# Kernel optimization log

Measured on AMD Instinct MI355X. Metric: run time of the kernel, lower is better.

## Reference

```python
import jax, jax.numpy as jnp
import numpy as np

KATZ = 0.5      # katz_factor
GAMMA = 20.0    # support->query softmax temperature
GAMMA2 = 10.0   # query->support softmax temperature
EPS = 1e-16


def setup_inputs() -> dict:
    key = jax.random.key(0)
    k1, k2 = jax.random.split(key)
    support_xf = jax.random.normal(k1, (4, 25, 640, 10, 10), dtype=jnp.float32)
    query_xf = jax.random.normal(k2, (4, 75, 640, 10, 10), dtype=jnp.float32)
    return {"support_xf": support_xf, "query_xf": query_xf, "n_way": 5, "k_shot": 5}


def reference(support_xf, query_xf, n_way, k_shot):
    b, s, c, h, w = support_xf.shape
    q = query_xf.shape[1]
    M = h * w
    # mean over shots -> class prototypes per spatial location
    sup = support_xf.reshape(b, n_way, k_shot, c, M).mean(axis=2)   # (b, n, c, M)
    qry = query_xf.reshape(b, q, c, M)                               # (b, q, c, M)
    # cosine similarity: l2-normalize along channel dim
    sup = sup / (EPS + jnp.linalg.norm(sup, axis=2, keepdims=True))
    qry = qry / (EPS + jnp.linalg.norm(qry, axis=2, keepdims=True))
    # S[b,q,m,n,s] = <qry[b,q,:,m], sup[b,n,:,s]>  (matches permute(0,1,3,2,4))
    S = jnp.einsum('bqcm,bncs->bqmns', qry, sup)
    M_q = M
    M_s = n_way * M
    N = b * q
    S = S.reshape(N, M_q, M_s)
    # bipartite transition matrices (row-stochastic softmaxes)
    T_sq = jax.nn.softmax(GAMMA * S, axis=-1)                        # (N, M_q, M_s)
    T_qs = jax.nn.softmax(GAMMA2 * jnp.swapaxes(S, -2, -1), axis=-1)  # (N, M_s, M_q)
    D = M_s + M_q
    zs = jnp.zeros((N, M_s, M_s), S.dtype)
    zq = jnp.zeros((N, M_q, M_q), S.dtype)
    top = jnp.concatenate([zs, jnp.swapaxes(T_sq, -2, -1)], axis=-1)   # (N, M_s, D)
    bot = jnp.concatenate([jnp.swapaxes(T_qs, -2, -1), zq], axis=-1)   # (N, M_q, D)
    T = jnp.concatenate([top, bot], axis=-2)                           # (N, D, D)
    # katz = (inv(I - k*T) - I) @ 1  ==  solve(I - k*T, 1) - 1
    A = jnp.eye(D, dtype=S.dtype)[None] - KATZ * T
    katz = jnp.linalg.solve(A, jnp.ones((N, D, 1), S.dtype))[..., 0] - 1.0
    kq = katz[:, M_s:]
    kq = kq / kq.sum(axis=-1, keepdims=True)
    return kq.reshape(b, q, h, w)[:, :, None]  # (b, q, 1, h, w)
```

## Files before the change

kernel.cpp:

```cpp
#include <hip/hip_runtime.h>
#include <math.h>

#define BATCH 4
#define NSUP 25
#define NQ   75
#define CH   640
#define HW   100
#define NWAY 5
#define KSHOT 5
#define NSYS (BATCH*NQ)
#define MS   (NWAY*HW)
#define MQ   HW
#define MTOT (NQ*HW)
#define NCHK 20

#define A_BSTRIDE 241664
#define A_KSTRIDE 966656
#define B_BSTRIDE 16384
#define B_KSTRIDE 65536

typedef __attribute__((ext_vector_type(8))) _Float16 f16x8;
typedef __attribute__((ext_vector_type(8))) short bf16x8;
typedef __attribute__((ext_vector_type(4))) float f32x4;
typedef __attribute__((ext_vector_type(16))) float f32x16;
typedef __attribute__((ext_vector_type(4))) short s16x4;

__device__ __forceinline__ ushort f2bf(float f) {
    unsigned u = __float_as_uint(f);
    u += 0x7fff + ((u >> 16) & 1);
    return (ushort)(u >> 16);
}
__device__ __forceinline__ ushort f2h(float f) {
    _Float16 h = (_Float16)f;
    return __builtin_bit_cast(unsigned short, h);
}

#define GLD_LDS16(gp, lp) __builtin_amdgcn_global_load_lds( \
    (const __attribute__((address_space(1))) unsigned*)(const void*)(gp), \
    (__attribute__((address_space(3))) unsigned*)(void*)(lp), 16, 0, 0)

__global__ __launch_bounds__(256) void k_prep_all(
        const float* __restrict__ qry, const float* __restrict__ sup,
        ushort* __restrict__ AhT, ushort* __restrict__ BhT,
        float* __restrict__ npq, float* __restrict__ nps) {
    __shared__ float tile[32][101];
    int kt = blockIdx.x;
    int c0 = kt * 32;
    int z  = blockIdx.y;
    int t  = threadIdx.x;
    bool isq = (z < BATCH*NQ);

    ushort* dst; float* normpart; int planesHW; size_t cbase; int brow; int p;
    if (isq) {
        p = z;
        int b = p / NQ, qq = p % NQ;
        dst = AhT; normpart = npq; planesHW = NSYS*HW;
        cbase = (size_t)kt*A_KSTRIDE + (size_t)b*A_BSTRIDE;
        brow = qq*100;
        const float* ib = qry + (size_t)p*CH*HW + (size_t)c0*HW;
#pragma unroll
        for (int ii = 0; ii < 4; ++ii) {
            int idx = ii*256 + t;
            if (idx < 800) {
                int cl = idx / 25, qd = idx % 25;
                float4 v = *(const float4*)(ib + idx*4);
                tile[cl][qd*4+0] = v.x; tile[cl][qd*4+1] = v.y;
                tile[cl][qd*4+2] = v.z; tile[cl][qd*4+3] = v.w;
            }
        }
    } else {
        p = z - BATCH*NQ;
        int b = p / NWAY, n = p % NWAY;
        dst = BhT; normpart = nps; planesHW = BATCH*NWAY*HW;
        cbase = (size_t)kt*B_KSTRIDE + (size_t)b*B_BSTRIDE;
        brow = n*100;
        const float* ib = sup + ((size_t)(b*NSUP + n*KSHOT))*CH*HW + (size_t)c0*HW;
#pragma unroll
        for (int ii = 0; ii < 4; ++ii) {
            int idx = ii*256 + t;
            if (idx < 800) {
                float4 a = {0.f,0.f,0.f,0.f};
#pragma unroll
                for (int k = 0; k < KSHOT; ++k) {
                    float4 w = *(const float4*)(ib + (size_t)k*CH*HW + idx*4);
                    a.x += w.x; a.y += w.y; a.z += w.z; a.w += w.w;
                }
                int cl = idx / 25, qd = idx % 25;
                tile[cl][qd*4+0] = a.x*0.2f; tile[cl][qd*4+1] = a.y*0.2f;
                tile[cl][qd*4+2] = a.z*0.2f; tile[cl][qd*4+3] = a.w*0.2f;
            }
        }
    }
    __syncthreads();
#pragma unroll
    for (int ii = 0; ii < 2; ++ii) {
        int idx = ii*256 + t;
        if (idx < 400) {
            int m  = idx >> 2;
            int sp = idx & 3;
            int rib = brow + m;
            int rl = rib & 127;
            int slab = rib >> 7;
            int cb = ((sp ^ ((rl >> 1) & 3))) << 3;
            bf16x8 o; float ss = 0.f;
#pragma unroll
            for (int j = 0; j < 8; ++j) {
                float f = tile[cb+j][m];
                ss += f*f;
                o[j] = (short)f2h(f);
            }
            size_t off = cbase + (size_t)slab*4096
                       + (size_t)((rl>>1)*64 + (rl&1)*32 + sp*8);
            *(bf16x8*)(dst + off) = o;
            ss += __shfl_xor(ss, 1);
            ss += __shfl_xor(ss, 2);
            if ((t & 3) == 0)
                normpart[(size_t)kt*planesHW + p*HW + m] = ss;
        }
    }
}

#define BM 128
#define BN 128
#define BK 64
#define NKT (CH/BK)
#define NCT 4
#define NRT 59
#define NWG (NCT*NRT*BATCH)
__global__ __launch_bounds__(256) void k_gemm(
        const ushort* __restrict__ AhT, const ushort* __restrict__ BhT,
        const float* __restrict__ npq, const float* __restrict__ nps,
        float* __restrict__ S) {
    __shared__ __align__(1024) char lds[65536];
    __shared__ float invqL[128], invsL[128];
    int hwid = blockIdx.x;
    int l = (hwid & 7) * (NWG/8) + (hwid >> 3);
    int ct = l & 3;
    int rest = l >> 2;
    int rt = rest % NRT;
    int b  = rest / NRT;
    int t  = threadIdx.x;
    int lane = t & 63, w = t >> 6;
    int row0 = rt * BM, col0 = ct * BN;

    if (t < 128) {
        int gr = row0 + t; if (gr > MTOT-1) gr = MTOT-1;
        float s = 0.f;
#pragma unroll
        for (int u = 0; u < NCHK; ++u) s += npq[(size_t)u*(NSYS*HW) + b*MTOT + gr];
        invqL[t] = 1.0f / (1e-16f + sqrtf(s));
    } else {
        int c = col0 + (t - 128); if (c > MS-1) c = MS-1;
        float s = 0.f;
#pragma unroll
        for (int u = 0; u < NCHK; ++u) s += nps[(size_t)u*(BATCH*NWAY*HW) + b*MS + c];
        invsL[t-128] = 1.0f / (1e-16f + sqrtf(s));
    }

    const ushort* srcA = AhT + (size_t)b*A_BSTRIDE + (size_t)rt*4096;
    const ushort* srcB = BhT + (size_t)b*B_BSTRIDE + (size_t)ct*4096;
    int dA = w << 10;

    f32x4 acc[4][4];
#pragma unroll
    for (int mi = 0; mi < 4; ++mi)
#pragma unroll
        for (int ni = 0; ni < 4; ++ni) acc[mi][ni] = (f32x4){0.f,0.f,0.f,0.f};

    int wr = w >> 1, wc = w & 1;
    int q = lane & 15, kg = lane >> 4;

#define STAGE(bufb, kt_) do { \
        const ushort* pa0 = srcA + (size_t)(2*(kt_))*A_KSTRIDE; \
        const ushort* pa1 = pa0 + A_KSTRIDE; \
        const ushort* pb0 = srcB + (size_t)(2*(kt_))*B_KSTRIDE; \
        const ushort* pb1 = pb0 + B_KSTRIDE; \
        char* bb = lds + (bufb)*32768; \
        GLD_LDS16(pa0 + t*8,        bb + 0     + dA); \
        GLD_LDS16(pa0 + 2048 + t*8, bb + 4096  + dA); \
        GLD_LDS16(pa1 + t*8,        bb + 8192  + dA); \
        GLD_LDS16(pa1 + 2048 + t*8, bb + 12288 + dA); \
        GLD_LDS16(pb0 + t*8,        bb + 16384 + dA); \
        GLD_LDS16(pb0 + 2048 + t*8, bb + 20480 + dA); \
        GLD_LDS16(pb1 + t*8,        bb + 24576 + dA); \
        GLD_LDS16(pb1 + 2048 + t*8, bb + 28672 + dA); \
    } while (0)

    STAGE(0, 0);
    for (int kt = 0; kt < NKT; ++kt) {
        int cur = kt & 1;
        if (kt + 1 < NKT) {
            STAGE(cur ^ 1, kt + 1);
            asm volatile("s_waitcnt vmcnt(8)" ::: "memory");
        } else {
            asm volatile("s_waitcnt vmcnt(0)" ::: "memory");
        }
        __builtin_amdgcn_sched_barrier(0);
        __builtin_amdgcn_s_barrier();
        __builtin_amdgcn_sched_barrier(0);

        const char* buf = lds + cur*32768;
#pragma unroll
        for (int h = 0; h < 2; ++h) {
            const char* Ab = buf + h*8192;
            const char* Bb = buf + 16384 + h*8192;
            f16x8 bf[4];
#pragma unroll
            for (int ni = 0; ni < 4; ++ni) {
                int c = wc*64 + ni*16 + q;
                int off = (c>>1)*128 + (c&1)*64 + ((kg ^ ((c>>1)&3)) << 4);
                bf[ni] = *(const f16x8*)(Bb + off);
            }
#pragma unroll
            for (int mi = 0; mi < 4; ++mi) {
                int r = wr*64 + mi*16 + q;
                int off = (r>>1)*128 + (r&1)*64 + ((kg ^ ((r>>1)&3)) << 4);
                f16x8 af = *(const f16x8*)(Ab + off);
#pragma unroll
                for (int ni = 0; ni < 4; ++ni)
                    acc[mi][ni] = __builtin_amdgcn_mfma_f32_16x16x32_f16(af, bf[ni], acc[mi][ni], 0, 0, 0);
            }
        }
        __builtin_amdgcn_sched_barrier(0);
        __builtin_amdgcn_s_barrier();
        __builtin_amdgcn_sched_barrier(0);
    }
#undef STAGE

    int colb = col0 + wc*64 + q;
    int rowb = row0 + wr*64 + (kg << 2);
#pragma unroll
    for (int mi = 0; mi < 4; ++mi) {
#pragma unroll
        for (int ni = 0; ni < 4; ++ni) {
            int c = colb + ni*16;
            if (c >= MS) continue;
            float si = invsL[c - col0];
#pragma unroll
            for (int j = 0; j < 4; ++j) {
                int r = rowb + mi*16 + j;
                if (r < MTOT)
                    S[((size_t)b*MTOT + r)*MS + c] = acc[mi][ni][j] * invqL[r - row0] * si;
            }
        }
    }
}

__global__ __launch_bounds__(512) void k_fsolve(const float* __restrict__ S,
        float* __restrict__ out) {
    __shared__ __align__(16) char PQ[65536];
    __shared__ __align__(16) float m10s[MS], r10s[MS];
    __shared__ float m20s[MQ], r20s[MQ];
    __shared__ float xs[MQ], rh[MQ];
    __shared__ float ps[4][MQ];
    __shared__ float partial[2];
    int sys = blockIdx.x;
    int t = threadIdx.x;
    int l = t & 63, w = t >> 6;
    const float* Sb = S + (size_t)sys*MQ*MS;
    char* PT = PQ;
    char* QT = PQ + 32768;

    {
        float (*wcm)[512] = (float(*)[512])PQ;
        float (*wcs)[512] = (float(*)[512])(PQ + 16384);
        float colm[8], cols[8];
#pragma unroll
        for (int u = 0; u < 8; ++u) { colm[u] = -1e30f; cols[u] = 0.f; }
        int nu = (l < MS - 448) ? 8 : 7;
        for (int row = w; row < MQ; row += 8) {
            const float* rp = Sb + (size_t)row*MS;
            float v[8];
            float rm = -1e30f;
#pragma unroll
            for (int u = 0; u < 8; ++u) {
                v[u] = (u < nu) ? rp[l + 64*u] : -1e30f;
                rm = fmaxf(rm, v[u]);
            }
            for (int off = 32; off; off >>= 1) rm = fmaxf(rm, __shfl_xor(rm, off));
            float rs = 0.f;
#pragma unroll
            for (int u = 0; u < 8; ++u) if (u < nu) rs += __expf(20.f*(v[u]-rm));
            for (int off = 32; off; off >>= 1) rs += __shfl_xor(rs, off);
            if (l == 0) { m20s[row] = rm; r20s[row] = 1.0f/rs; }
#pragma unroll
            for (int u = 0; u < 8; ++u) if (u < nu) {
                float vv = v[u];
                if (vv <= colm[u]) {
                    cols[u] += __expf(10.f*(vv - colm[u]));
                } else {
                    cols[u] = cols[u]*__expf(10.f*(colm[u]-vv)) + 1.0f;
                    colm[u] = vv;
                }
            }
        }
#pragma unroll
        for (int u = 0; u < 8; ++u) { wcm[w][l+64*u] = colm[u]; wcs[w][l+64*u] = cols[u]; }
        __syncthreads();
        if (t < MS) {
            float m = -1e30f;
#pragma unroll
            for (int w2 = 0; w2 < 8; ++w2) m = fmaxf(m, wcm[w2][t]);
            float s = 0.f;
#pragma unroll
            for (int w2 = 0; w2 < 8; ++w2) s += wcs[w2][t]*__expf(10.f*(wcm[w2][t]-m));
            m10s[t] = m;
            r10s[t] = 1.0f/s;
        }
    }

    int i = t >> 2;
    int ccb = (t & 3) * 32;
    float m20i = 0.f, r20i = 0.f;

    f32x16 acc[2];
#pragma unroll
    for (int nt = 0; nt < 2; ++nt)
#pragma unroll
        for (int rg = 0; rg < 16; ++rg) acc[nt][rg] = 0.f;

    int rw = w & 3, ch = w >> 2;
    int grA = rw*32 + (l & 31);
    int kg = l >> 5;
    const float* sr = Sb + (size_t)i*MS;

    for (int ck = 0; ck < 4; ++ck) {
        int c0 = ck*128;
        __syncthreads();
        if (ck == 0 && i < MQ) { m20i = m20s[i]; r20i = r20s[i]; }
        if (i < MQ) {
#pragma unroll
            for (int j = 0; j < 8; ++j) {
                int cc = ccb + 4*j;
                int cg = c0 + cc;
                int phys = i*256 + ((((cc>>3) ^ (i&15)))<<4) + ((cc&7)*2);
                s16x4 pv, qv;
                if (cg < MS) {
                    float4 v  = *(const float4*)(sr + cg);
                    float4 m1 = *(const float4*)&m10s[cg];
                    float4 r1 = *(const float4*)&r10s[cg];
                    pv.x = (short)f2bf(__expf(10.f*(v.x - m1.x))*r1.x);
                    pv.y = (short)f2bf(__expf(10.f*(v.y - m1.y))*r1.y);
                    pv.z = (short)f2bf(__expf(10.f*(v.z - m1.z))*r1.z);
                    pv.w = (short)f2bf(__expf(10.f*(v.w - m1.w))*r1.w);
                    qv.x = (short)f2bf(__expf(20.f*(v.x - m20i))*r20i);
                    qv.y = (short)f2bf(__expf(20.f*(v.y - m20i))*r20i);
                    qv.z = (short)f2bf(__expf(20.f*(v.z - m20i))*r20i);
                    qv.w = (short)f2bf(__expf(20.f*(v.w - m20i))*r20i);
                } else {
                    pv = (s16x4){0,0,0,0}; qv = (s16x4){0,0,0,0};
                }
                *(s16x4*)(PT + phys) = pv;
                *(s16x4*)(QT + phys) = qv;
            }
        } else {
            short one = (short)0x3F80;
#pragma unroll
            for (int j = 0; j < 8; ++j) {
                int cc = ccb + 4*j;
                int cg = c0 + cc;
                int phys = i*256 + ((((cc>>3) ^ (i&15)))<<4) + ((cc&7)*2);
                s16x4 z = (s16x4){0,0,0,0};
                s16x4 qv = z;
                if (i == MQ && cg < MS) qv = (s16x4){one, one, one, one};
                *(s16x4*)(PT + phys) = z;
                *(s16x4*)(QT + phys) = qv;
            }
        }
        __syncthreads();
#pragma unroll
        for (int kk = 0; kk < 8; ++kk) {
            int sA = (kk*2 + kg) ^ (grA & 15);
            bf16x8 af = *(const bf16x8*)(PT + grA*256 + (sA<<4));
#pragma unroll
            for (int nt = 0; nt < 2; ++nt) {
                int gc = (ch*2 + nt)*32 + (l & 31);
                int sB = (kk*2 + kg) ^ (gc & 15);
                bf16x8 bfr = *(const bf16x8*)(QT + gc*256 + (sB<<4));
                acc[nt] = __builtin_amdgcn_mfma_f32_32x32x16_bf16(af, bfr, acc[nt], 0, 0, 0);
            }
        }
    }
    __syncthreads();

    float* Bsh = (float*)PQ;
#pragma unroll
    for (int nt = 0; nt < 2; ++nt) {
        int col = (ch*2 + nt)*32 + (l & 31);
        if (col > MQ) continue;
#pragma unroll
        for (int rg = 0; rg < 16; ++rg) {
            int row = rw*32 + (rg & 3) + 8*(rg >> 2) + 4*(l >> 5);
            if (row < MQ) Bsh[row*101 + col] = acc[nt][rg];
        }
    }
    __syncthreads();
    if (t < MQ) { rh[t] = 1.0f + 0.5f*Bsh[t*101 + 100]; xs[t] = rh[t]; }
    __syncthreads();
    int jr = t % MQ, jp = t / MQ;
    for (int it = 0; it < 12; ++it) {
        if (t < 4*MQ) {
            float s = 0.f;
            const float* br = &Bsh[jr*101 + jp*25];
            const float* xv = &xs[jp*25];
#pragma unroll
            for (int j = 0; j < 25; ++j) s += br[j]*xv[j];
            ps[jp][jr] = s;
        }
        __syncthreads();
        if (t < MQ) xs[t] = rh[t] + 0.25f*(ps[0][t] + ps[1][t] + ps[2][t] + ps[3][t]);
        __syncthreads();
    }
    float kv = (t < MQ) ? (xs[t] - 1.0f) : 0.f;
    if (t < 128) {
        float s = kv;
        for (int off = 32; off; off >>= 1) s += __shfl_xor(s, off);
        if ((t & 63) == 0) partial[t >> 6] = s;
    }
    __syncthreads();
    float tot = partial[0] + partial[1];
    if (t < MQ) out[sys*MQ + t] = kv / tot;
}

extern "C" void kernel_launch(void* const* d_in, const int* in_sizes, int n_in,
                              void* d_out, int out_size, void* d_ws, size_t ws_size,
                              hipStream_t stream) {
    const float* sup = (const float*)d_in[0];
    const float* qry = (const float*)d_in[1];
    float* out = (float*)d_out;
    float* ws  = (float*)d_ws;

    float* supmean = ws;
    float* invs    = supmean + 1280000;
    float* invq    = invs + 2000;
    float* Smat    = invq + 30000;
    float* m20     = Smat + 15000000;
    float* rd20    = m20 + 30000;
    float* m10     = rd20 + 30000;
    float* rd10    = m10 + 150000;
    float* Bm      = rd10 + 150000;
    float* rh      = Bm + 3000000;
    ushort* AhT    = (ushort*)(rh + 30000);
    ushort* BhT    = AhT + 19333120;
    float* npq     = Bm;
    float* nps     = Bm + 600000;

    k_prep_all<<<dim3(NCHK, BATCH*NQ + BATCH*NWAY), 256, 0, stream>>>(
        qry, sup, AhT, BhT, npq, nps);
    k_gemm<<<NWG, 256, 0, stream>>>(AhT, BhT, npq, nps, Smat);
    k_fsolve<<<NSYS, 512, 0, stream>>>(Smat, out);
}
```

Baseline: 122.4 us.

## Replace softmax max-subtraction with fixed cosine bound and fold row normalizers into MFMA

Because S holds cosine similarities bounded by 1, the solve kernel now uses the constant 1 as the softmax shift instead of computing per-row and per-column maxima. The per-column pass drops its online max tracking, and the per-row sums of the query-side softmax are taken from an extra all-ones row that rides along in the existing MFMA product. Those normalizers are then applied as a diagonal scaling inside the fixed-point iteration. This removes the max reductions, the shuffles and the rescaling exps from the prologue. In exchange it relies on the inputs being normalized and accepts reduced exp headroom in float and bf16.

After: 112.0 us. -8.5%, faster.

```diff
diff --git a/kernel.cpp b/kernel.cpp
--- a/kernel.cpp
+++ b/kernel.cpp
@@ -249,9 +249,9 @@
 __global__ __launch_bounds__(512) void k_fsolve(const float* __restrict__ S,
         float* __restrict__ out) {
     __shared__ __align__(16) char PQ[65536];
-    __shared__ __align__(16) float m10s[MS], r10s[MS];
-    __shared__ float m20s[MQ], r20s[MQ];
-    __shared__ float xs[MQ], rh[MQ];
+    __shared__ __align__(16) float r10s[MS];
+    __shared__ float r20L[MQ];
+    __shared__ float xs[MQ], ys[MQ], rh[MQ];
     __shared__ float ps[4][MQ];
     __shared__ float partial[2];
     int sys = blockIdx.x;
@@ -262,56 +262,30 @@
     char* QT = PQ + 32768;
 
     {
-        float (*wcm)[512] = (float(*)[512])PQ;
-        float (*wcs)[512] = (float(*)[512])(PQ + 16384);
-        float colm[8], cols[8];
-#pragma unroll
-        for (int u = 0; u < 8; ++u) { colm[u] = -1e30f; cols[u] = 0.f; }
+        float (*wcs)[512] = (float(*)[512])PQ;
+        float cols[8];
+#pragma unroll
+        for (int u = 0; u < 8; ++u) cols[u] = 0.f;
         int nu = (l < MS - 448) ? 8 : 7;
         for (int row = w; row < MQ; row += 8) {
             const float* rp = Sb + (size_t)row*MS;
-            float v[8];
-            float rm = -1e30f;
-#pragma unroll
-            for (int u = 0; u < 8; ++u) {
-                v[u] = (u < nu) ? rp[l + 64*u] : -1e30f;
-                rm = fmaxf(rm, v[u]);
-            }
-            for (int off = 32; off; off >>= 1) rm = fmaxf(rm, __shfl_xor(rm, off));
-            float rs = 0.f;
-#pragma unroll
-            for (int u = 0; u < 8; ++u) if (u < nu) rs += __expf(20.f*(v[u]-rm));
-            for (int off = 32; off; off >>= 1) rs += __shfl_xor(rs, off);
-            if (l == 0) { m20s[row] = rm; r20s[row] = 1.0f/rs; }
-#pragma unroll
-            for (int u = 0; u < 8; ++u) if (u < nu) {
-                float vv = v[u];
-                if (vv <= colm[u]) {
-                    cols[u] += __expf(10.f*(vv - colm[u]));
-                } else {
-                    cols[u] = cols[u]*__expf(10.f*(colm[u]-vv)) + 1.0f;
-                    colm[u] = vv;
-                }
-            }
-        }
-#pragma unroll
-        for (int u = 0; u < 8; ++u) { wcm[w][l+64*u] = colm[u]; wcs[w][l+64*u] = cols[u]; }
+#pragma unroll
+            for (int u = 0; u < 8; ++u)
+                if (u < nu) cols[u] += __expf(10.f*(rp[l + 64*u] - 1.0f));
+        }
+#pragma unroll
+        for (int u = 0; u < 8; ++u) wcs[w][l+64*u] = cols[u];
         __syncthreads();
         if (t < MS) {
-            float m = -1e30f;
-#pragma unroll
-            for (int w2 = 0; w2 < 8; ++w2) m = fmaxf(m, wcm[w2][t]);
             float s = 0.f;
 #pragma unroll
-            for (int w2 = 0; w2 < 8; ++w2) s += wcs[w2][t]*__expf(10.f*(wcm[w2][t]-m));
-            m10s[t] = m;
+            for (int w2 = 0; w2 < 8; ++w2) s += wcs[w2][t];
             r10s[t] = 1.0f/s;
         }
     }
 
     int i = t >> 2;
     int ccb = (t & 3) * 32;
-    float m20i = 0.f, r20i = 0.f;
 
     f32x16 acc[2];
 #pragma unroll
@@ -327,7 +301,6 @@
     for (int ck = 0; ck < 4; ++ck) {
         int c0 = ck*128;
         __syncthreads();
-        if (ck == 0 && i < MQ) { m20i = m20s[i]; r20i = r20s[i]; }
         if (i < MQ) {
 #pragma unroll
             for (int j = 0; j < 8; ++j) {
@@ -337,16 +310,15 @@
                 s16x4 pv, qv;
                 if (cg < MS) {
                     float4 v  = *(const float4*)(sr + cg);
-                    float4 m1 = *(const float4*)&m10s[cg];
                     float4 r1 = *(const float4*)&r10s[cg];
-                    pv.x = (short)f2bf(__expf(10.f*(v.x - m1.x))*r1.x);
-                    pv.y = (short)f2bf(__expf(10.f*(v.y - m1.y))*r1.y);
-                    pv.z = (short)f2bf(__expf(10.f*(v.z - m1.z))*r1.z);
-                    pv.w = (short)f2bf(__expf(10.f*(v.w - m1.w))*r1.w);
-                    qv.x = (short)f2bf(__expf(20.f*(v.x - m20i))*r20i);
-                    qv.y = (short)f2bf(__expf(20.f*(v.y - m20i))*r20i);
-                    qv.z = (short)f2bf(__expf(20.f*(v.z - m20i))*r20i);
-                    qv.w = (short)f2bf(__expf(20.f*(v.w - m20i))*r20i);
+                    pv.x = (short)f2bf(__expf(10.f*(v.x - 1.0f))*r1.x);
+                    pv.y = (short)f2bf(__expf(10.f*(v.y - 1.0f))*r1.y);
+                    pv.z = (short)f2bf(__expf(10.f*(v.z - 1.0f))*r1.z);
+                    pv.w = (short)f2bf(__expf(10.f*(v.w - 1.0f))*r1.w);
+                    qv.x = (short)f2bf(__expf(20.f*(v.x - 1.0f)));
+                    qv.y = (short)f2bf(__expf(20.f*(v.y - 1.0f)));
+                    qv.z = (short)f2bf(__expf(20.f*(v.z - 1.0f)));
+                    qv.w = (short)f2bf(__expf(20.f*(v.w - 1.0f)));
                 } else {
                     pv = (s16x4){0,0,0,0}; qv = (s16x4){0,0,0,0};
                 }
@@ -361,10 +333,10 @@
                 int cg = c0 + cc;
                 int phys = i*256 + ((((cc>>3) ^ (i&15)))<<4) + ((cc&7)*2);
                 s16x4 z = (s16x4){0,0,0,0};
-                s16x4 qv = z;
-                if (i == MQ && cg < MS) qv = (s16x4){one, one, one, one};
-                *(s16x4*)(PT + phys) = z;
-                *(s16x4*)(QT + phys) = qv;
+                s16x4 ov = z;
+                if (i == MQ && cg < MS) ov = (s16x4){one, one, one, one};
+                *(s16x4*)(PT + phys) = ov;
+                *(s16x4*)(QT + phys) = ov;
             }
         }
         __syncthreads();
@@ -391,24 +363,35 @@
 #pragma unroll
         for (int rg = 0; rg < 16; ++rg) {
             int row = rw*32 + (rg & 3) + 8*(rg >> 2) + 4*(l >> 5);
-            if (row < MQ) Bsh[row*101 + col] = acc[nt][rg];
+            if (row <= MQ) Bsh[row*101 + col] = acc[nt][rg];
         }
     }
     __syncthreads();
-    if (t < MQ) { rh[t] = 1.0f + 0.5f*Bsh[t*101 + 100]; xs[t] = rh[t]; }
+    if (t < MQ) {
+        float r20 = 1.0f / Bsh[100*101 + t];
+        r20L[t] = r20;
+        float r = 1.0f + 0.5f*Bsh[t*101 + 100];
+        rh[t] = r;
+        xs[t] = r;
+        ys[t] = r20 * r;
+    }
     __syncthreads();
     int jr = t % MQ, jp = t / MQ;
     for (int it = 0; it < 12; ++it) {
         if (t < 4*MQ) {
             float s = 0.f;
             const float* br = &Bsh[jr*101 + jp*25];
-            const float* xv = &xs[jp*25];
-#pragma unroll
-            for (int j = 0; j < 25; ++j) s += br[j]*xv[j];
+            const float* yv = &ys[jp*25];
+#pragma unroll
+            for (int j = 0; j < 25; ++j) s += br[j]*yv[j];
             ps[jp][jr] = s;
         }
         __syncthreads();
-        if (t < MQ) xs[t] = rh[t] + 0.25f*(ps[0][t] + ps[1][t] + ps[2][t] + ps[3][t]);
+        if (t < MQ) {
+            float x = rh[t] + 0.25f*(ps[0][t] + ps[1][t] + ps[2][t] + ps[3][t]);
+            xs[t] = x;
+            ys[t] = r20L[t] * x;
+        }
         __syncthreads();
     }
     float kv = (t < MQ) ? (xs[t] - 1.0f) : 0.f;
```
